# Optimization experiments

Measured on AMD Instinct MI355X. Metric: run time of the kernel, lower is better.

Reference implementation:

```python
import jax, jax.numpy as jnp
import numpy as np

N = 20000      # nodes
E = 320000     # edges (before self-loops)
G = 64         # graphs in batch
IN = 128       # in_channels
HID = 64       # hidden_dim
NEG_SLOPE = 0.2


def setup_inputs() -> dict:
    key = jax.random.key(0)
    ks = jax.random.split(key, 20)
    def glorot(k, shape):
        fan = shape[0] + shape[-1]
        return jax.random.normal(k, shape, jnp.float32) * np.sqrt(2.0 / fan)
    inp = {
        'x': jax.random.normal(ks[0], (N, IN), jnp.float32),
        'edge_index': jax.random.randint(ks[1], (2, E), 0, N, jnp.int32),
        'batch': jnp.sort(jax.random.randint(ks[2], (N,), 0, G, jnp.int32)),
        # GAT layer 1: heads=4, out=64, concat=False
        'W1': glorot(ks[3], (IN, 4 * HID)),
        'as1': glorot(ks[4], (4, HID)),
        'ad1': glorot(ks[5], (4, HID)),
        'b1': jnp.zeros((HID,), jnp.float32),
        # GAT layer 2: heads=2, out=32, concat=False
        'W2': glorot(ks[6], (HID, 2 * (HID // 2))),
        'as2': glorot(ks[7], (2, HID // 2)),
        'ad2': glorot(ks[8], (2, HID // 2)),
        'b2': jnp.zeros((HID // 2,), jnp.float32),
        # continue head: 32->16->1
        'cW1': glorot(ks[9], (HID // 2, HID // 4)), 'cb1': jnp.zeros((HID // 4,), jnp.float32),
        'cW2': glorot(ks[10], (HID // 4, 1)), 'cb2': jnp.zeros((1,), jnp.float32),
        # halt head: 32->16->1
        'hW1': glorot(ks[11], (HID // 2, HID // 4)), 'hb1': jnp.zeros((HID // 4,), jnp.float32),
        'hW2': glorot(ks[12], (HID // 4, 1)), 'hb2': jnp.zeros((1,), jnp.float32),
    }
    return inp


def gat_layer(x, src, dst, W, att_src, att_dst, bias, heads, out_ch):
    # x: [N, Fin] -> h: [N, H, C]
    n = x.shape[0]
    h = (x @ W).reshape(n, heads, out_ch)
    a_src = jnp.einsum('nhc,hc->nh', h, att_src)   # [N, H]
    a_dst = jnp.einsum('nhc,hc->nh', h, att_dst)   # [N, H]
    e = jax.nn.leaky_relu(a_src[src] + a_dst[dst], NEG_SLOPE)   # [E', H]
    # segment softmax over incoming edges of each dst node
    m = jax.ops.segment_max(e, dst, num_segments=n)             # [N, H]
    ee = jnp.exp(e - m[dst])
    denom = jax.ops.segment_sum(ee, dst, num_segments=n)        # [N, H]
    alpha = ee / (denom[dst] + 1e-16)                           # [E', H]
    msg = h[src] * alpha[:, :, None]                            # [E', H, C]
    out = jax.ops.segment_sum(msg, dst, num_segments=n)         # [N, H, C]
    return out.mean(axis=1) + bias                              # concat=False -> head mean


def reference(x, edge_index, batch, W1, as1, ad1, b1, W2, as2, ad2, b2,
              cW1, cb1, cW2, cb2, hW1, hb1, hW2, hb2):
    n = x.shape[0]
    loop = jnp.arange(n, dtype=edge_index.dtype)
    src = jnp.concatenate([edge_index[0], loop])   # add self-loops (PyG default)
    dst = jnp.concatenate([edge_index[1], loop])

    h1 = jax.nn.relu(gat_layer(x, src, dst, W1, as1, ad1, b1, 4, HID))
    h2 = jax.nn.relu(gat_layer(h1, src, dst, W2, as2, ad2, b2, 2, HID // 2))

    # global mean pool per graph
    sums = jax.ops.segment_sum(h2, batch, num_segments=G)                 # [G, 32]
    cnt = jax.ops.segment_sum(jnp.ones((n,), h2.dtype), batch, num_segments=G)
    emb = sums / jnp.maximum(cnt, 1.0)[:, None]                           # [G, 32]

    cont = jax.nn.sigmoid(jax.nn.relu(emb @ cW1 + cb1) @ cW2 + cb2)       # [G, 1]
    halt = jax.nn.sigmoid(jax.nn.relu(emb @ hW1 + hb1) @ hW2 + hb2)       # [G, 1]
    return (halt, cont)
```

## Files before the change

kernel.cpp:

```cpp
#include <hip/hip_runtime.h>
#include <hip/hip_fp16.h>


#define G_GRAPHS 64

using half8   = __attribute__((ext_vector_type(8))) _Float16;
using half4v  = __attribute__((ext_vector_type(4))) _Float16;
using floatx4 = __attribute__((ext_vector_type(4))) float;
using floatx2 = __attribute__((ext_vector_type(2))) float;

__global__ __launch_bounds__(256) void zero_deg(int4* __restrict__ deg4, int n4)
{
    int i = blockIdx.x * 256 + threadIdx.x;
    if (i < n4) deg4[i] = int4{0, 0, 0, 0};
}

__global__ __launch_bounds__(256) void ell_gemm1(
        const int* __restrict__ ei, int* __restrict__ deg16,
        int* __restrict__ col_ell, int E0, int Etot, int mb,
        const float* __restrict__ A, const float* __restrict__ B,
        unsigned char* __restrict__ C8, const float* __restrict__ att_s,
        const float* __restrict__ att_d, float* __restrict__ a_s,
        float* __restrict__ a_d, int M)
{
    __shared__ _Float16 As[64][136];
    __shared__ _Float16 Bt[64][136];

    if ((int)blockIdx.x >= mb) {
        int idx = ((int)blockIdx.x - mb) * 256 + threadIdx.x;
        if (idx < Etot) {
            int src = (idx < E0) ? ei[idx]      : (idx - E0);
            int dst = (idx < E0) ? ei[E0 + idx] : (idx - E0);
            int slot = atomicAdd(&deg16[dst << 4], 1);
            if (slot < 64)
                col_ell[(size_t)dst * 64 + slot] = src;
        }
        return;
    }

    const int tid  = threadIdx.x;
    const int row0 = blockIdx.x * 64;
    const int wid  = tid >> 6;
    const int lane = tid & 63;
    const int r    = lane & 15;
    const int quad = lane >> 4;
    const int rw0  = wid * 16;

    const int arow = tid >> 2;
    const int akc  = (tid & 3) * 32;
    const int agr  = row0 + arow;

    #pragma unroll
    for (int i = 0; i < 4; i++) {
        half8 v = {};
        if (agr < M) {
            const float* p = &A[(size_t)agr * 128 + akc + i * 8];
            float4 f0 = *reinterpret_cast<const float4*>(p);
            float4 f1 = *reinterpret_cast<const float4*>(p + 4);
            v[0] = (_Float16)f0.x; v[1] = (_Float16)f0.y;
            v[2] = (_Float16)f0.z; v[3] = (_Float16)f0.w;
            v[4] = (_Float16)f1.x; v[5] = (_Float16)f1.y;
            v[6] = (_Float16)f1.z; v[7] = (_Float16)f1.w;
        }
        *reinterpret_cast<half8*>(&As[arow][akc + i * 8]) = v;
    }

    for (int by = 0; by < 4; by++) {
        __syncthreads();

        #pragma unroll
        for (int i = 0; i < 8; i++) {
            int id = tid + 256 * i;
            int k  = id >> 4;
            int n4 = (id & 15) * 4;
            float4 f = *reinterpret_cast<const float4*>(
                &B[(size_t)k * 256 + by * 64 + n4]);
            Bt[n4 + 0][k] = (_Float16)f.x;
            Bt[n4 + 1][k] = (_Float16)f.y;
            Bt[n4 + 2][k] = (_Float16)f.z;
            Bt[n4 + 3][k] = (_Float16)f.w;
        }
        __syncthreads();

        floatx4 acc[4] = {};
        #pragma unroll
        for (int s = 0; s < 4; s++) {
            half8 af = *reinterpret_cast<const half8*>(&As[rw0 + r][s * 32 + quad * 8]);
            #pragma unroll
            for (int nt = 0; nt < 4; nt++) {
                half8 bf = *reinterpret_cast<const half8*>(&Bt[nt * 16 + r][s * 32 + quad * 8]);
                acc[nt] = __builtin_amdgcn_mfma_f32_16x16x32_f16(af, bf, acc[nt], 0, 0, 0);
            }
        }

        float ps[4], pd[4];
        #pragma unroll
        for (int reg = 0; reg < 4; reg++) { ps[reg] = 0.f; pd[reg] = 0.f; }
        #pragma unroll
        for (int nt = 0; nt < 4; nt++) {
            int cl = nt * 16 + r;
            float ws = att_s[by * 64 + cl];
            float wd = att_d[by * 64 + cl];
            #pragma unroll
            for (int reg = 0; reg < 4; reg++) {
                ps[reg] += acc[nt][reg] * ws;
                pd[reg] += acc[nt][reg] * wd;
            }
        }
        #pragma unroll
        for (int off = 1; off < 16; off <<= 1)
            #pragma unroll
            for (int reg = 0; reg < 4; reg++) {
                ps[reg] += __shfl_xor(ps[reg], off);
                pd[reg] += __shfl_xor(pd[reg], off);
            }
        if (r == 0) {
            #pragma unroll
            for (int reg = 0; reg < 4; reg++) {
                int gr = row0 + rw0 + quad * 4 + reg;
                if (gr < M) {
                    a_s[gr * 4 + by] = ps[reg];
                    a_d[gr * 4 + by] = pd[reg];
                }
            }
        }

        __syncthreads();
        unsigned char (*lds8)[80] = reinterpret_cast<unsigned char(*)[80]>(&Bt[0][0]);
        #pragma unroll
        for (int nt = 0; nt < 4; nt++) {
            #pragma unroll
            for (int reg = 0; reg < 4; reg++) {
                int wv = __builtin_amdgcn_cvt_pk_fp8_f32(
                    acc[nt][reg], acc[nt][reg], 0, false);
                lds8[rw0 + quad * 4 + reg][nt * 16 + r] = (unsigned char)(wv & 0xFF);
            }
        }
        __syncthreads();
        {
            int row = tid >> 2;
            int c16 = (tid & 3) * 16;
            int gr  = row0 + row;
            if (gr < M) {
                int4 v = *reinterpret_cast<const int4*>(&lds8[row][c16]);
                *reinterpret_cast<int4*>(&C8[(size_t)gr * 256 + by * 64 + c16]) = v;
            }
        }
    }
}

template<int K, int HPB, bool A_FP32, bool B_FP32>
__device__ __forceinline__ void gemm_att_tile(
        const void* __restrict__ A_v, const void* __restrict__ B_v,
        void* __restrict__ C_out, const float* __restrict__ att_s,
        const float* __restrict__ att_d, float* __restrict__ a_s,
        float* __restrict__ a_d, int M, int Ntot, int Htot,
        int row0, int col0, int by,
        _Float16 (*As)[K + 8], _Float16 (*Bt)[K + 8])
{
    constexpr int CPH = 64 / HPB;
    constexpr int NTH = 4 / HPB;
    const int tid = threadIdx.x;

    {
        int row = tid >> 2;
        int kc  = (tid & 3) * (K / 4);
        int gr  = row0 + row;
        #pragma unroll
        for (int i = 0; i < K / 32; i++) {
            half8 v = {};
            if (gr < M) {
                if constexpr (A_FP32) {
                    const float* Af = (const float*)A_v;
                    float4 f0 = *reinterpret_cast<const float4*>(&Af[(size_t)gr * K + kc + i * 8]);
                    float4 f1 = *reinterpret_cast<const float4*>(&Af[(size_t)gr * K + kc + i * 8 + 4]);
                    v[0] = (_Float16)f0.x; v[1] = (_Float16)f0.y;
                    v[2] = (_Float16)f0.z; v[3] = (_Float16)f0.w;
                    v[4] = (_Float16)f1.x; v[5] = (_Float16)f1.y;
                    v[6] = (_Float16)f1.z; v[7] = (_Float16)f1.w;
                } else {
                    const _Float16* Ah = (const _Float16*)A_v;
                    v = *reinterpret_cast<const half8*>(&Ah[(size_t)gr * K + kc + i * 8]);
                }
            }
            *reinterpret_cast<half8*>(&As[row][kc + i * 8]) = v;
        }
    }
    {
        #pragma unroll
        for (int i = 0; i < K / 16; i++) {
            int id = tid + 256 * i;
            int k  = id >> 4;
            int n4 = (id & 15) * 4;
            _Float16 b0, b1, b2, b3;
            if constexpr (B_FP32) {
                const float* Bf = (const float*)B_v;
                float4 f = *reinterpret_cast<const float4*>(&Bf[(size_t)k * Ntot + col0 + n4]);
                b0 = (_Float16)f.x; b1 = (_Float16)f.y;
                b2 = (_Float16)f.z; b3 = (_Float16)f.w;
            } else {
                const _Float16* Bh = (const _Float16*)B_v;
                half4v v = *reinterpret_cast<const half4v*>(&Bh[(size_t)k * Ntot + col0 + n4]);
                b0 = v[0]; b1 = v[1]; b2 = v[2]; b3 = v[3];
            }
            Bt[n4 + 0][k] = b0; Bt[n4 + 1][k] = b1;
            Bt[n4 + 2][k] = b2; Bt[n4 + 3][k] = b3;
        }
    }
    __syncthreads();

    const int wid  = tid >> 6;
    const int lane = tid & 63;
    const int r    = lane & 15;
    const int quad = lane >> 4;
    const int rw0  = wid * 16;

    floatx4 acc[4] = {};
    #pragma unroll
    for (int s = 0; s < K / 32; s++) {
        half8 af = *reinterpret_cast<const half8*>(&As[rw0 + r][s * 32 + quad * 8]);
        #pragma unroll
        for (int nt = 0; nt < 4; nt++) {
            half8 bf = *reinterpret_cast<const half8*>(&Bt[nt * 16 + r][s * 32 + quad * 8]);
            acc[nt] = __builtin_amdgcn_mfma_f32_16x16x32_f16(af, bf, acc[nt], 0, 0, 0);
        }
    }

    float ps[HPB][4], pd[HPB][4];
    #pragma unroll
    for (int hl = 0; hl < HPB; hl++)
        #pragma unroll
        for (int reg = 0; reg < 4; reg++) { ps[hl][reg] = 0.f; pd[hl][reg] = 0.f; }

    #pragma unroll
    for (int nt = 0; nt < 4; nt++) {
        int hl = nt / NTH;
        int cl = (nt % NTH) * 16 + r;
        int hglob = by * HPB + hl;
        float ws = att_s[hglob * CPH + cl];
        float wd = att_d[hglob * CPH + cl];
        #pragma unroll
        for (int reg = 0; reg < 4; reg++) {
            ps[hl][reg] += acc[nt][reg] * ws;
            pd[hl][reg] += acc[nt][reg] * wd;
        }
    }
    #pragma unroll
    for (int off = 1; off < 16; off <<= 1)
        #pragma unroll
        for (int hl = 0; hl < HPB; hl++)
            #pragma unroll
            for (int reg = 0; reg < 4; reg++) {
                ps[hl][reg] += __shfl_xor(ps[hl][reg], off);
                pd[hl][reg] += __shfl_xor(pd[hl][reg], off);
            }
    if (r == 0) {
        #pragma unroll
        for (int reg = 0; reg < 4; reg++) {
            int gr = row0 + rw0 + quad * 4 + reg;
            if (gr < M) {
                #pragma unroll
                for (int hl = 0; hl < HPB; hl++) {
                    int hglob = by * HPB + hl;
                    a_s[gr * Htot + hglob] = ps[hl][reg];
                    a_d[gr * Htot + hglob] = pd[hl][reg];
                }
            }
        }
    }

    _Float16* Ch = (_Float16*)C_out;
    #pragma unroll
    for (int nt = 0; nt < 4; nt++) {
        #pragma unroll
        for (int reg = 0; reg < 4; reg++) {
            int gr = row0 + rw0 + quad * 4 + reg;
            if (gr < M)
                Ch[(size_t)gr * Ntot + col0 + nt * 16 + r] = (_Float16)acc[nt][reg];
        }
    }
}

__global__ __launch_bounds__(256) void gemm2_kernel(
        const _Float16* __restrict__ A, const float* __restrict__ B,
        _Float16* __restrict__ Ch, const float* __restrict__ att_s,
        const float* __restrict__ att_d, float* __restrict__ a_s,
        float* __restrict__ a_d, int M)
{
    __shared__ _Float16 As[64][72];
    __shared__ _Float16 Bt[64][72];
    gemm_att_tile<64, 2, false, true>(
        A, B, Ch, att_s, att_d, a_s, a_d,
        M, 64, 2, blockIdx.x * 64, 0, 0, As, Bt);
}

__device__ inline void facc4_h(float* a, float2 raw, float p) {
    __half2 h0 = *reinterpret_cast<__half2*>(&raw.x);
    __half2 h1 = *reinterpret_cast<__half2*>(&raw.y);
    float2 f0 = __half22float2(h0), f1 = __half22float2(h1);
    a[0] += p * f0.x; a[1] += p * f0.y; a[2] += p * f1.x; a[3] += p * f1.y;
}
__device__ inline void facc4_8(float* a, unsigned int w, float p) {
    floatx2 lo = __builtin_amdgcn_cvt_pk_f32_fp8((int)w, false);
    floatx2 hi = __builtin_amdgcn_cvt_pk_f32_fp8((int)w, true);
    a[0] += p * lo[0]; a[1] += p * lo[1]; a[2] += p * hi[0]; a[3] += p * hi[1];
}
__device__ inline void facc8_8(float* a, uint2 w, float p) {
    facc4_8(a,     w.x, p);
    facc4_8(a + 4, w.y, p);
}

template<int H, int C, bool OUT_HALF, bool FEAT_FP8>
__device__ void gat_general(
        int d, int lo, int degc, const int* __restrict__ colidx,
        const void* __restrict__ hfeat_v, const float* __restrict__ a_s,
        const float* __restrict__ a_d, const float* __restrict__ bias,
        void* __restrict__ out_v, int N, float* p_wave)
{
    if (d >= N) return;
    constexpr int FV = (H * C) / 64;
    const int lane = threadIdx.x & 63;
    const int hi = lo + degc;
    const __half* hfeat = (const __half*)hfeat_v;
    const unsigned char* ffeat = (const unsigned char*)hfeat_v;
    const int h_lane = (lane * FV) / C;

    float adp[H];
    #pragma unroll
    for (int h = 0; h < H; h++) adp[h] = a_d[d * H + h];
    float lh[H];
    #pragma unroll
    for (int h = 0; h < H; h++) lh[h] = 0.f;
    float acc[FV];
    #pragma unroll
    for (int v = 0; v < FV; v++) acc[v] = 0.f;

    float mh[H];
    #pragma unroll
    for (int h = 0; h < H; h++) mh[h] = -3.0e38f;
    for (int i = lo + lane; i < hi; i += 64) {
        int s = colidx[i];
        #pragma unroll
        for (int h = 0; h < H; h++) {
            float v = a_s[s * H + h] + adp[h];
            v = (v > 0.f) ? v : 0.2f * v;
            mh[h] = fmaxf(mh[h], v);
        }
    }
    #pragma unroll
    for (int off = 1; off < 64; off <<= 1)
        #pragma unroll
        for (int h = 0; h < H; h++)
            mh[h] = fmaxf(mh[h], __shfl_xor(mh[h], off));

    for (int base = lo; base < hi; base += 64) {
        int i = base + lane;
        int s = 0;
        if (i < hi) {
            s = colidx[i];
            #pragma unroll
            for (int h = 0; h < H; h++) {
                float v = a_s[s * H + h] + adp[h];
                v = (v > 0.f) ? v : 0.2f * v;
                float p = __expf(v - mh[h]);
                lh[h] += p;
                p_wave[(i - base) * H + h] = p;
            }
        }
        int cnt = min(64, hi - base);
        for (int j = 0; j < cnt; j++) {
            int s_j = __shfl(s, j);
            float pj = p_wave[j * H + h_lane];
            if constexpr (FV == 4 && FEAT_FP8) {
                unsigned int raw = *reinterpret_cast<const unsigned int*>(
                    ffeat + (size_t)s_j * (H * C) + lane * 4);
                facc4_8(acc, raw, pj);
            } else if constexpr (FV == 4) {
                float2 raw = *reinterpret_cast<const float2*>(
                    hfeat + (size_t)s_j * (H * C) + lane * 4);
                facc4_h(acc, raw, pj);
            } else {
                acc[0] += pj * __half2float(hfeat[(size_t)s_j * (H * C) + lane]);
            }
        }
    }
    #pragma unroll
    for (int off = 1; off < 64; off <<= 1)
        #pragma unroll
        for (int h = 0; h < H; h++)
            lh[h] += __shfl_xor(lh[h], off);

    float lsel = lh[0];
    #pragma unroll
    for (int h = 1; h < H; h++) if (h_lane == h) lsel = lh[h];
    const float inv = 1.0f / (lsel + 1e-16f);

    if constexpr (FV == 4) {
        float vx = acc[0] * inv, vy = acc[1] * inv,
              vz = acc[2] * inv, vw = acc[3] * inv;
        vx += __shfl_xor(vx, 16); vy += __shfl_xor(vy, 16);
        vz += __shfl_xor(vz, 16); vw += __shfl_xor(vw, 16);
        vx += __shfl_xor(vx, 32); vy += __shfl_xor(vy, 32);
        vz += __shfl_xor(vz, 32); vw += __shfl_xor(vw, 32);
        if (lane < 16) {
            float4 bv = *reinterpret_cast<const float4*>(&bias[lane * 4]);
            float ox = fmaxf(0.25f * vx + bv.x, 0.f);
            float oy = fmaxf(0.25f * vy + bv.y, 0.f);
            float oz = fmaxf(0.25f * vz + bv.z, 0.f);
            float ow = fmaxf(0.25f * vw + bv.w, 0.f);
            if constexpr (OUT_HALF) {
                half4v hv = { (_Float16)ox, (_Float16)oy, (_Float16)oz, (_Float16)ow };
                *reinterpret_cast<half4v*>((_Float16*)out_v + (size_t)d * C + lane * 4) = hv;
            } else {
                float4 o = make_float4(ox, oy, oz, ow);
                *reinterpret_cast<float4*>((float*)out_v + (size_t)d * C + lane * 4) = o;
            }
        }
    } else {
        float v = acc[0] * inv;
        v += __shfl_xor(v, 32);
        if (lane < 32) {
            float o = fmaxf(0.5f * v + bias[lane], 0.f);
            if constexpr (OUT_HALF)
                ((_Float16*)out_v)[(size_t)d * C + lane] = (_Float16)o;
            else
                ((float*)out_v)[(size_t)d * C + lane] = o;
        }
    }
}

template<int H, int C, bool OUT_HALF, bool FEAT_FP8>
__global__ __launch_bounds__(256) void gat_dst(
        const int* __restrict__ degv, const int* __restrict__ col_ell,
        const void* __restrict__ hfeat_v, const float* __restrict__ a_s,
        const float* __restrict__ a_d, const float* __restrict__ bias,
        void* __restrict__ out_v, int N)
{
    const int wid  = threadIdx.x >> 6;
    const int lane = threadIdx.x & 63;
    const int nw   = lane >> 5;
    const int l32  = lane & 31;

    __shared__ float p_sh[4][64 * H];

    const int d  = blockIdx.x * 8 + wid * 2 + nw;
    const bool nodeok = (d < N);
    const int lo = d * 64;

    int degc = 0;
    if (nodeok) degc = min(degv[d << 4], 64);
    const int degA = __shfl(degc, 0);
    const int degB = __shfl(degc, 32);
    const bool fast = (degA <= 32) && (degB <= 32);

    if (fast) {
        const __half* hfeat = (const __half*)hfeat_v;
        const unsigned char* ffeat = (const unsigned char*)hfeat_v;

        float adp[H];
        #pragma unroll
        for (int h = 0; h < H; h++) adp[h] = nodeok ? a_d[d * H + h] : 0.f;

        int s = 0;
        float lh[H];
        #pragma unroll
        for (int h = 0; h < H; h++) lh[h] = 0.f;
        const bool valid = nodeok && (l32 < degc);
        if (valid) {
            s = col_ell[lo + l32];
            if constexpr (H == 4) {
                float4 av = *reinterpret_cast<const float4*>(&a_s[s * 4]);
                float ev[4] = {av.x + adp[0], av.y + adp[1],
                               av.z + adp[2], av.w + adp[3]};
                #pragma unroll
                for (int h = 0; h < 4; h++) {
                    float e = (ev[h] > 0.f) ? ev[h] : 0.2f * ev[h];
                    float p = __expf(e);
                    lh[h] = p;
                    p_sh[wid][nw * 32 * H + l32 * H + h] = p;
                }
            } else {
                float2 av = *reinterpret_cast<const float2*>(&a_s[s * 2]);
                float ev[2] = {av.x + adp[0], av.y + adp[1]};
                #pragma unroll
                for (int h = 0; h < 2; h++) {
                    float e = (ev[h] > 0.f) ? ev[h] : 0.2f * ev[h];
                    float p = __expf(e);
                    lh[h] = p;
                    p_sh[wid][nw * 32 * H + l32 * H + h] = p;
                }
            }
        }
        #pragma unroll
        for (int off = 1; off < 32; off <<= 1)
            #pragma unroll
            for (int h = 0; h < H; h++)
                lh[h] += __shfl_xor(lh[h], off);

        const int sbase = nw * 32;

        if constexpr (H == 4) {
            const int hl = l32 >> 3;
            float a0[8] = {}, a1[8] = {};
            int j = 0;
            for (; j + 8 <= degc; j += 8) {
                uint2 raw[8]; float pw[8];
                #pragma unroll
                for (int u = 0; u < 8; u++) {
                    int sj = __shfl(s, sbase + j + u);
                    pw[u]  = p_sh[wid][nw * 128 + (j + u) * 4 + hl];
                    raw[u] = *reinterpret_cast<const uint2*>(
                        ffeat + (size_t)sj * 256 + l32 * 8);
                }
                #pragma unroll
                for (int u = 0; u < 8; u++)
                    facc8_8((u & 1) ? a1 : a0, raw[u], pw[u]);
            }
            for (; j < degc; j++) {
                int sj = __shfl(s, sbase + j);
                float pw = p_sh[wid][nw * 128 + j * 4 + hl];
                uint2 raw = *reinterpret_cast<const uint2*>(
                    ffeat + (size_t)sj * 256 + l32 * 8);
                facc8_8(a0, raw, pw);
            }
            #pragma unroll
            for (int k = 0; k < 8; k++) a0[k] += a1[k];

            float lsel = lh[0];
            #pragma unroll
            for (int h = 1; h < 4; h++) if (hl == h) lsel = lh[h];
            float inv = 1.0f / (lsel + 1e-16f);
            #pragma unroll
            for (int k = 0; k < 8; k++) {
                float v = a0[k] * inv;
                v += __shfl_xor(v, 8);
                v += __shfl_xor(v, 16);
                a0[k] = v;
            }
            if (nodeok && l32 < 8) {
                float4 b0 = *reinterpret_cast<const float4*>(&bias[l32 * 8]);
                float4 b1 = *reinterpret_cast<const float4*>(&bias[l32 * 8 + 4]);
                float bb[8] = {b0.x, b0.y, b0.z, b0.w, b1.x, b1.y, b1.z, b1.w};
                half8 hv;
                #pragma unroll
                for (int k = 0; k < 8; k++)
                    hv[k] = (_Float16)fmaxf(0.25f * a0[k] + bb[k], 0.f);
                *reinterpret_cast<half8*>((_Float16*)out_v + (size_t)d * 64 + l32 * 8) = hv;
            }
        } else {
            const int q   = l32 >> 4;
            const int l16 = l32 & 15;
            const int hl2 = l16 >> 3;
            float a0[4] = {}, a1[4] = {};
            int j = 0;
            for (; j + 8 <= degc; j += 8) {
                float2 raw[4]; float pw[4];
                #pragma unroll
                for (int u = 0; u < 4; u++) {
                    int je = j + 2 * u + q;
                    int sj = __shfl(s, sbase + je);
                    pw[u]  = p_sh[wid][nw * 64 + je * 2 + hl2];
                    raw[u] = *reinterpret_cast<const float2*>(
                        (const _Float16*)hfeat + (size_t)sj * 64 + l16 * 4);
                }
                #pragma unroll
                for (int u = 0; u < 4; u++)
                    facc4_h((u & 1) ? a1 : a0, raw[u], pw[u]);
            }
            for (int jr = j + q; jr < degc; jr += 2) {
                int sj = __shfl(s, sbase + jr);
                float pw = p_sh[wid][nw * 64 + jr * 2 + hl2];
                float2 raw = *reinterpret_cast<const float2*>(
                    (const _Float16*)hfeat + (size_t)sj * 64 + l16 * 4);
                facc4_h(a0, raw, pw);
            }
            #pragma unroll
            for (int k = 0; k < 4; k++) {
                a0[k] += a1[k];
                a0[k] += __shfl_xor(a0[k], 16);
            }
            float lsel = (hl2 == 0) ? lh[0] : lh[1];
            float inv = 1.0f / (lsel + 1e-16f);
            #pragma unroll
            for (int k = 0; k < 4; k++) {
                float v = a0[k] * inv;
                v += __shfl_xor(v, 8);
                a0[k] = v;
            }
            if (nodeok && l32 < 8) {
                float4 bb = *reinterpret_cast<const float4*>(&bias[l32 * 4]);
                float4 o;
                o.x = fmaxf(0.5f * a0[0] + bb.x, 0.f);
                o.y = fmaxf(0.5f * a0[1] + bb.y, 0.f);
                o.z = fmaxf(0.5f * a0[2] + bb.z, 0.f);
                o.w = fmaxf(0.5f * a0[3] + bb.w, 0.f);
                *reinterpret_cast<float4*>((float*)out_v + (size_t)d * 32 + l32 * 4) = o;
            }
        }
        return;
    }

    const int dA = blockIdx.x * 8 + wid * 2;
    gat_general<H, C, OUT_HALF, FEAT_FP8>(
        dA, dA * 64, __shfl(degc, 0), col_ell,
        hfeat_v, a_s, a_d, bias, out_v, N, p_sh[wid]);
    gat_general<H, C, OUT_HALF, FEAT_FP8>(
        dA + 1, (dA + 1) * 64, __shfl(degc, 32), col_ell,
        hfeat_v, a_s, a_d, bias, out_v, N, p_sh[wid]);
}

__global__ __launch_bounds__(256) void pool_heads(
        const float* __restrict__ h2, const int* __restrict__ batch,
        const float* __restrict__ cW1, const float* __restrict__ cb1,
        const float* __restrict__ cW2, const float* __restrict__ cb2,
        const float* __restrict__ hW1, const float* __restrict__ hb1,
        const float* __restrict__ hW2, const float* __restrict__ hb2,
        float* __restrict__ out, int N)
{
    const int g = blockIdx.x;
    const int c = threadIdx.x & 31;
    const int r = threadIdx.x >> 5;

    __shared__ int bounds[2];
    __shared__ float red[8][32];
    __shared__ float emb_s[32];
    __shared__ float hidden[32];

    if (threadIdx.x < 2) {
        int target = g + (int)threadIdx.x;
        int lo = 0, hi = N;
        while (lo < hi) {
            int mid = (lo + hi) >> 1;
            if (batch[mid] < target) lo = mid + 1; else hi = mid;
        }
        bounds[threadIdx.x] = lo;
    }
    __syncthreads();
    const int lo = bounds[0], hi = bounds[1];

    float acc = 0.f;
    for (int n = lo + r; n < hi; n += 8)
        acc += h2[(size_t)n * 32 + c];
    red[r][c] = acc;
    __syncthreads();
    if (r == 0) {
        float s = 0.f;
        #pragma unroll
        for (int i = 0; i < 8; i++) s += red[i][c];
        emb_s[c] = s / fmaxf((float)(hi - lo), 1.0f);
    }
    __syncthreads();

    if (threadIdx.x < 32) {
        int j = threadIdx.x & 15;
        bool is_halt = threadIdx.x >= 16;
        const float* w1v = is_halt ? hW1 : cW1;
        const float* b1v = is_halt ? hb1 : cb1;
        const float* w2v = is_halt ? hW2 : cW2;
        float s = b1v[j];
        #pragma unroll
        for (int cc = 0; cc < 32; cc++) s += emb_s[cc] * w1v[cc * 16 + j];
        hidden[threadIdx.x] = fmaxf(s, 0.f) * w2v[j];
    }
    __syncthreads();
    if (threadIdx.x == 0) {
        float sc = cb2[0], sh = hb2[0];
        #pragma unroll
        for (int i = 0; i < 16; i++) { sc += hidden[i]; sh += hidden[16 + i]; }
        out[g]            = 1.0f / (1.0f + __expf(-sh));
        out[G_GRAPHS + g] = 1.0f / (1.0f + __expf(-sc));
    }
}

extern "C" void kernel_launch(void* const* d_in, const int* in_sizes, int n_in,
                              void* d_out, int out_size, void* d_ws, size_t ws_size,
                              hipStream_t stream)
{
    const float* x   = (const float*)d_in[0];
    const int*   ei  = (const int*)  d_in[1];
    const int*   bat = (const int*)  d_in[2];
    const float* W1  = (const float*)d_in[3];
    const float* as1 = (const float*)d_in[4];
    const float* ad1 = (const float*)d_in[5];
    const float* b1  = (const float*)d_in[6];
    const float* W2  = (const float*)d_in[7];
    const float* as2 = (const float*)d_in[8];
    const float* ad2 = (const float*)d_in[9];
    const float* b2  = (const float*)d_in[10];
    const float* cW1 = (const float*)d_in[11];
    const float* cb1 = (const float*)d_in[12];
    const float* cW2 = (const float*)d_in[13];
    const float* cb2 = (const float*)d_in[14];
    const float* hW1 = (const float*)d_in[15];
    const float* hb1 = (const float*)d_in[16];
    const float* hW2 = (const float*)d_in[17];
    const float* hb2 = (const float*)d_in[18];

    const int N    = in_sizes[2];
    const int E0   = in_sizes[1] / 2;
    const int Etot = E0 + N;

    float* w = (float*)d_ws;
    size_t o = 0;
    unsigned char* h1pre_f8 = (unsigned char*)(w + o); o += (size_t)N * 64;
    _Float16* h1_h    = (_Float16*)(w + o); o += (size_t)N * 32;
    _Float16* h2pre_h = (_Float16*)(w + o); o += (size_t)N * 32;
    float* a_s1  = w + o; o += (size_t)N * 4;
    float* a_d1  = w + o; o += (size_t)N * 4;
    float* a_s2  = w + o; o += (size_t)N * 2;
    float* a_d2  = w + o; o += (size_t)N * 2;
    float* h2    = w + o; o += (size_t)N * 32;
    int* deg16   = (int*)(w + o); o += (size_t)N * 16;
    int* col_ell = (int*)(w + o); o += (size_t)N * 64;
    (void)ws_size; (void)n_in; (void)out_size;

    const dim3 blk(256);
    const int eb  = (Etot + 255) / 256;
    const int nb8 = (N + 7) / 8;
    const int mb  = (N + 63) / 64;

    const int n4 = N * 4;
    zero_deg<<<(n4 + 255) / 256, blk, 0, stream>>>((int4*)deg16, n4);

    ell_gemm1<<<mb + eb, blk, 0, stream>>>(
        ei, deg16, col_ell, E0, Etot, mb,
        x, W1, h1pre_f8, as1, ad1, a_s1, a_d1, N);

    gat_dst<4, 64, true, true><<<nb8, blk, 0, stream>>>(
        deg16, col_ell, h1pre_f8, a_s1, a_d1, b1, h1_h, N);

    gemm2_kernel<<<mb, blk, 0, stream>>>(
        h1_h, W2, h2pre_h, as2, ad2, a_s2, a_d2, N);
    gat_dst<2, 32, false, false><<<nb8, blk, 0, stream>>>(
        deg16, col_ell, h2pre_h, a_s2, a_d2, b2, h2, N);

    pool_heads<<<G_GRAPHS, blk, 0, stream>>>(
        h2, bat, cW1, cb1, cW2, cb2, hW1, hb1, hW2, hb2, (float*)d_out, N);
}
```

Before: 106.2 us.

## Process four destination nodes per wave in layer-1 GAT aggregation with 16-byte loads

Adds a dedicated layer-1 aggregation kernel that maps 16 lanes per destination node instead of 32, so each wave handles four nodes and each lane loads 16 fp8 features (uint4) per neighbour. Each lane computes attention weights for two edges, which halves the number of blocks launched. The aim is fewer, wider memory transactions and more nodes in flight per wave, in exchange for doubled accumulator registers (32 floats) that may lower occupancy. The generic gat_dst template is simplified to only the H=2 path used by layer 2.

```diff
diff --git a/kernel.cpp b/kernel.cpp
--- a/kernel.cpp
+++ b/kernel.cpp
@@ -308,6 +308,12 @@
 __device__ inline void facc8_8(float* a, uint2 w, float p) {
     facc4_8(a,     w.x, p);
     facc4_8(a + 4, w.y, p);
+}
+__device__ inline void facc16_8(float* a, uint4 w, float p) {
+    facc4_8(a,      w.x, p);
+    facc4_8(a + 4,  w.y, p);
+    facc4_8(a + 8,  w.z, p);
+    facc4_8(a + 12, w.w, p);
 }
 
 template<int H, int C, bool OUT_HALF, bool FEAT_FP8>
@@ -429,6 +435,142 @@
     }
 }
 
+__global__ __launch_bounds__(256) void gat1_v2(
+        const int* __restrict__ degv, const int* __restrict__ col_ell,
+        const unsigned char* __restrict__ ffeat,
+        const float* __restrict__ a_s, const float* __restrict__ a_d,
+        const float* __restrict__ bias, _Float16* __restrict__ out, int N)
+{
+    const int wid  = threadIdx.x >> 6;
+    const int lane = threadIdx.x & 63;
+    const int nq   = lane >> 4;
+    const int l16  = lane & 15;
+
+    __shared__ float p_sh[16][128];
+
+    const int nodeIdx = wid * 4 + nq;
+    const int d  = blockIdx.x * 16 + nodeIdx;
+    const bool nodeok = (d < N);
+    const int lo = d * 64;
+
+    int degc = 0;
+    if (nodeok) degc = min(degv[d << 4], 64);
+    const int d0 = __shfl(degc, 0), d1 = __shfl(degc, 16);
+    const int d2 = __shfl(degc, 32), d3 = __shfl(degc, 48);
+    const bool fast = (max(max(d0, d1), max(d2, d3)) <= 32);
+
+    if (fast) {
+        float adp[4];
+        if (nodeok) {
+            float4 ad4 = *reinterpret_cast<const float4*>(&a_d[d * 4]);
+            adp[0] = ad4.x; adp[1] = ad4.y; adp[2] = ad4.z; adp[3] = ad4.w;
+        } else {
+            adp[0] = adp[1] = adp[2] = adp[3] = 0.f;
+        }
+
+        int s0 = 0, s1 = 0;
+        float lh[4] = {0.f, 0.f, 0.f, 0.f};
+        if (nodeok && l16 < degc) {
+            s0 = col_ell[lo + l16];
+            float4 av = *reinterpret_cast<const float4*>(&a_s[s0 * 4]);
+            float ev[4] = {av.x + adp[0], av.y + adp[1],
+                           av.z + adp[2], av.w + adp[3]};
+            float4 pv;
+            #pragma unroll
+            for (int h = 0; h < 4; h++) {
+                float e = (ev[h] > 0.f) ? ev[h] : 0.2f * ev[h];
+                float p = __expf(e);
+                lh[h] += p;
+                ((float*)&pv)[h] = p;
+            }
+            *reinterpret_cast<float4*>(&p_sh[nodeIdx][l16 * 4]) = pv;
+        }
+        if (nodeok && 16 + l16 < degc) {
+            s1 = col_ell[lo + 16 + l16];
+            float4 av = *reinterpret_cast<const float4*>(&a_s[s1 * 4]);
+            float ev[4] = {av.x + adp[0], av.y + adp[1],
+                           av.z + adp[2], av.w + adp[3]};
+            float4 pv;
+            #pragma unroll
+            for (int h = 0; h < 4; h++) {
+                float e = (ev[h] > 0.f) ? ev[h] : 0.2f * ev[h];
+                float p = __expf(e);
+                lh[h] += p;
+                ((float*)&pv)[h] = p;
+            }
+            *reinterpret_cast<float4*>(&p_sh[nodeIdx][(16 + l16) * 4]) = pv;
+        }
+        #pragma unroll
+        for (int off = 1; off < 16; off <<= 1)
+            #pragma unroll
+            for (int h = 0; h < 4; h++)
+                lh[h] += __shfl_xor(lh[h], off);
+
+        const int sb   = nq * 16;
+        const int hsel = l16 >> 2;
+        const int coff = l16 * 16;
+        float a0[16] = {}, a1[16] = {};
+        int j = 0;
+        for (; j + 8 <= degc; j += 8) {
+            uint4 raw[8]; float pw[8];
+            #pragma unroll
+            for (int u = 0; u < 8; u++) {
+                int je = j + u;
+                int sj = (je < 16) ? __shfl(s0, sb + je)
+                                   : __shfl(s1, sb + je - 16);
+                pw[u]  = p_sh[nodeIdx][je * 4 + hsel];
+                raw[u] = *reinterpret_cast<const uint4*>(
+                    ffeat + (size_t)sj * 256 + coff);
+            }
+            #pragma unroll
+            for (int u = 0; u < 8; u++)
+                facc16_8((u & 1) ? a1 : a0, raw[u], pw[u]);
+        }
+        for (; j < degc; j++) {
+            int sj = (j < 16) ? __shfl(s0, sb + j)
+                              : __shfl(s1, sb + j - 16);
+            float pw = p_sh[nodeIdx][j * 4 + hsel];
+            uint4 raw = *reinterpret_cast<const uint4*>(
+                ffeat + (size_t)sj * 256 + coff);
+            facc16_8(a0, raw, pw);
+        }
+        #pragma unroll
+        for (int k = 0; k < 16; k++) a0[k] += a1[k];
+
+        float lsel = lh[0];
+        if (hsel == 1) lsel = lh[1];
+        if (hsel == 2) lsel = lh[2];
+        if (hsel == 3) lsel = lh[3];
+        float inv = 1.0f / (lsel + 1e-16f);
+        #pragma unroll
+        for (int k = 0; k < 16; k++) {
+            float v = a0[k] * inv;
+            v += __shfl_xor(v, 4);
+            v += __shfl_xor(v, 8);
+            a0[k] = v;
+        }
+        if (nodeok && l16 < 4) {
+            half8 hv0, hv1;
+            #pragma unroll
+            for (int k = 0; k < 8; k++) {
+                hv0[k] = (_Float16)fmaxf(0.25f * a0[k]     + bias[l16 * 16 + k],     0.f);
+                hv1[k] = (_Float16)fmaxf(0.25f * a0[8 + k] + bias[l16 * 16 + 8 + k], 0.f);
+            }
+            _Float16* op = out + (size_t)d * 64 + l16 * 16;
+            *reinterpret_cast<half8*>(op)     = hv0;
+            *reinterpret_cast<half8*>(op + 8) = hv1;
+        }
+        return;
+    }
+
+    const int dA = blockIdx.x * 16 + wid * 4;
+    const int dg[4] = {d0, d1, d2, d3};
+    for (int t = 0; t < 4; t++)
+        gat_general<4, 64, true, true>(
+            dA + t, (dA + t) * 64, dg[t], col_ell,
+            ffeat, a_s, a_d, bias, out, N, &p_sh[wid * 4][0]);
+}
+
 template<int H, int C, bool OUT_HALF, bool FEAT_FP8>
 __global__ __launch_bounds__(256) void gat_dst(
         const int* __restrict__ degv, const int* __restrict__ col_ell,
@@ -455,7 +597,6 @@
 
     if (fast) {
         const __half* hfeat = (const __half*)hfeat_v;
-        const unsigned char* ffeat = (const unsigned char*)hfeat_v;
 
         float adp[H];
         #pragma unroll
@@ -468,27 +609,14 @@
         const bool valid = nodeok && (l32 < degc);
         if (valid) {
             s = col_ell[lo + l32];
-            if constexpr (H == 4) {
-                float4 av = *reinterpret_cast<const float4*>(&a_s[s * 4]);
-                float ev[4] = {av.x + adp[0], av.y + adp[1],
-                               av.z + adp[2], av.w + adp[3]};
-                #pragma unroll
-                for (int h = 0; h < 4; h++) {
-                    float e = (ev[h] > 0.f) ? ev[h] : 0.2f * ev[h];
-                    float p = __expf(e);
-                    lh[h] = p;
-                    p_sh[wid][nw * 32 * H + l32 * H + h] = p;
-                }
-            } else {
-                float2 av = *reinterpret_cast<const float2*>(&a_s[s * 2]);
-                float ev[2] = {av.x + adp[0], av.y + adp[1]};
-                #pragma unroll
-                for (int h = 0; h < 2; h++) {
-                    float e = (ev[h] > 0.f) ? ev[h] : 0.2f * ev[h];
-                    float p = __expf(e);
-                    lh[h] = p;
-                    p_sh[wid][nw * 32 * H + l32 * H + h] = p;
-                }
+            float2 av = *reinterpret_cast<const float2*>(&a_s[s * 2]);
+            float ev[2] = {av.x + adp[0], av.y + adp[1]};
+            #pragma unroll
+            for (int h = 0; h < 2; h++) {
+                float e = (ev[h] > 0.f) ? ev[h] : 0.2f * ev[h];
+                float p = __expf(e);
+                lh[h] = p;
+                p_sh[wid][nw * 32 * H + l32 * H + h] = p;
             }
         }
         #pragma unroll
@@ -499,103 +627,53 @@
 
         const int sbase = nw * 32;
 
-        if constexpr (H == 4) {
-            const int hl = l32 >> 3;
-            float a0[8] = {}, a1[8] = {};
-            int j = 0;
-            for (; j + 8 <= degc; j += 8) {
-                uint2 raw[8]; float pw[8];
-                #pragma unroll
-                for (int u = 0; u < 8; u++) {
-                    int sj = __shfl(s, sbase + j + u);
-                    pw[u]  = p_sh[wid][nw * 128 + (j + u) * 4 + hl];
-                    raw[u] = *reinterpret_cast<const uint2*>(
-                        ffeat + (size_t)sj * 256 + l32 * 8);
-                }
-                #pragma unroll
-                for (int u = 0; u < 8; u++)
-                    facc8_8((u & 1) ? a1 : a0, raw[u], pw[u]);
-            }
-            for (; j < degc; j++) {
-                int sj = __shfl(s, sbase + j);
-                float pw = p_sh[wid][nw * 128 + j * 4 + hl];
-                uint2 raw = *reinterpret_cast<const uint2*>(
-                    ffeat + (size_t)sj * 256 + l32 * 8);
-                facc8_8(a0, raw, pw);
-            }
-            #pragma unroll
-            for (int k = 0; k < 8; k++) a0[k] += a1[k];
-
-            float lsel = lh[0];
-            #pragma unroll
-            for (int h = 1; h < 4; h++) if (hl == h) lsel = lh[h];
-            float inv = 1.0f / (lsel + 1e-16f);
-            #pragma unroll
-            for (int k = 0; k < 8; k++) {
-                float v = a0[k] * inv;
-                v += __shfl_xor(v, 8);
-                v += __shfl_xor(v, 16);
-                a0[k] = v;
-            }
-            if (nodeok && l32 < 8) {
-                float4 b0 = *reinterpret_cast<const float4*>(&bias[l32 * 8]);
-                float4 b1 = *reinterpret_cast<const float4*>(&bias[l32 * 8 + 4]);
-                float bb[8] = {b0.x, b0.y, b0.z, b0.w, b1.x, b1.y, b1.z, b1.w};
-                half8 hv;
-                #pragma unroll
-                for (int k = 0; k < 8; k++)
-                    hv[k] = (_Float16)fmaxf(0.25f * a0[k] + bb[k], 0.f);
-                *reinterpret_cast<half8*>((_Float16*)out_v + (size_t)d * 64 + l32 * 8) = hv;
-            }
-        } else {
-            const int q   = l32 >> 4;
-            const int l16 = l32 & 15;
-            const int hl2 = l16 >> 3;
-            float a0[4] = {}, a1[4] = {};
-            int j = 0;
-            for (; j + 8 <= degc; j += 8) {
-                float2 raw[4]; float pw[4];
-                #pragma unroll
-                for (int u = 0; u < 4; u++) {
-                    int je = j + 2 * u + q;
-                    int sj = __shfl(s, sbase + je);
-                    pw[u]  = p_sh[wid][nw * 64 + je * 2 + hl2];
-                    raw[u] = *reinterpret_cast<const float2*>(
-                        (const _Float16*)hfeat + (size_t)sj * 64 + l16 * 4);
-                }
-                #pragma unroll
-                for (int u = 0; u < 4; u++)
-                    facc4_h((u & 1) ? a1 : a0, raw[u], pw[u]);
-            }
-            for (int jr = j + q; jr < degc; jr += 2) {
-                int sj = __shfl(s, sbase + jr);
-                float pw = p_sh[wid][nw * 64 + jr * 2 + hl2];
-                float2 raw = *reinterpret_cast<const float2*>(
+        const int q   = l32 >> 4;
+        const int l16 = l32 & 15;
+        const int hl2 = l16 >> 3;
+        float a0[4] = {}, a1[4] = {};
+        int j = 0;
+        for (; j + 8 <= degc; j += 8) {
+            float2 raw[4]; float pw[4];
+            #pragma unroll
+            for (int u = 0; u < 4; u++) {
+                int je = j + 2 * u + q;
+                int sj = __shfl(s, sbase + je);
+                pw[u]  = p_sh[wid][nw * 64 + je * 2 + hl2];
+                raw[u] = *reinterpret_cast<const float2*>(
                     (const _Float16*)hfeat + (size_t)sj * 64 + l16 * 4);
-                facc4_h(a0, raw, pw);
-            }
-            #pragma unroll
-            for (int k = 0; k < 4; k++) {
-                a0[k] += a1[k];
-                a0[k] += __shfl_xor(a0[k], 16);
-            }
-            float lsel = (hl2 == 0) ? lh[0] : lh[1];
-            float inv = 1.0f / (lsel + 1e-16f);
-            #pragma unroll
-            for (int k = 0; k < 4; k++) {
-                float v = a0[k] * inv;
-                v += __shfl_xor(v, 8);
-                a0[k] = v;
-            }
-            if (nodeok && l32 < 8) {
-                float4 bb = *reinterpret_cast<const float4*>(&bias[l32 * 4]);
-                float4 o;
-                o.x = fmaxf(0.5f * a0[0] + bb.x, 0.f);
-                o.y = fmaxf(0.5f * a0[1] + bb.y, 0.f);
-                o.z = fmaxf(0.5f * a0[2] + bb.z, 0.f);
-                o.w = fmaxf(0.5f * a0[3] + bb.w, 0.f);
-                *reinterpret_cast<float4*>((float*)out_v + (size_t)d * 32 + l32 * 4) = o;
-            }
+            }
+            #pragma unroll
+            for (int u = 0; u < 4; u++)
+                facc4_h((u & 1) ? a1 : a0, raw[u], pw[u]);
+        }
+        for (int jr = j + q; jr < degc; jr += 2) {
+            int sj = __shfl(s, sbase + jr);
+            float pw = p_sh[wid][nw * 64 + jr * 2 + hl2];
+            float2 raw = *reinterpret_cast<const float2*>(
+                (const _Float16*)hfeat + (size_t)sj * 64 + l16 * 4);
+            facc4_h(a0, raw, pw);
+        }
+        #pragma unroll
+        for (int k = 0; k < 4; k++) {
+            a0[k] += a1[k];
+            a0[k] += __shfl_xor(a0[k], 16);
+        }
+        float lsel = (hl2 == 0) ? lh[0] : lh[1];
+        float inv = 1.0f / (lsel + 1e-16f);
+        #pragma unroll
+        for (int k = 0; k < 4; k++) {
+            float v = a0[k] * inv;
+            v += __shfl_xor(v, 8);
+            a0[k] = v;
+        }
+        if (nodeok && l32 < 8) {
+            float4 bb = *reinterpret_cast<const float4*>(&bias[l32 * 4]);
+            float4 o;
+            o.x = fmaxf(0.5f * a0[0] + bb.x, 0.f);
+            o.y = fmaxf(0.5f * a0[1] + bb.y, 0.f);
+            o.z = fmaxf(0.5f * a0[2] + bb.z, 0.f);
+            o.w = fmaxf(0.5f * a0[3] + bb.w, 0.f);
+            *reinterpret_cast<float4*>((float*)out_v + (size_t)d * 32 + l32 * 4) = o;
         }
         return;
     }
@@ -715,9 +793,10 @@
     (void)ws_size; (void)n_in; (void)out_size;
 
     const dim3 blk(256);
-    const int eb  = (Etot + 255) / 256;
-    const int nb8 = (N + 7) / 8;
-    const int mb  = (N + 63) / 64;
+    const int eb   = (Etot + 255) / 256;
+    const int nb8  = (N + 7) / 8;
+    const int nb16 = (N + 15) / 16;
+    const int mb   = (N + 63) / 64;
 
     const int n4 = N * 4;
     zero_deg<<<(n4 + 255) / 256, blk, 0, stream>>>((int4*)deg16, n4);
@@ -726,7 +805,7 @@
         ei, deg16, col_ell, E0, Etot, mb,
         x, W1, h1pre_f8, as1, ad1, a_s1, a_d1, N);
 
-    gat_dst<4, 64, true, true><<<nb8, blk, 0, stream>>>(
+    gat1_v2<<<nb16, blk, 0, stream>>>(
         deg16, col_ell, h1pre_f8, a_s1, a_d1, b1, h1_h, N);
 
     gemm2_kernel<<<mb, blk, 0, stream>>>(
```

Result: slower. 121.4 us (+14.3%).
